# Kernel tuning notes

Measured on AMD Instinct MI355X. Metric: run time of the kernel, lower is better.

The kernel has to match this reference:

```python
import jax, jax.numpy as jnp
import numpy as np

VOCAB = 100000
DIM = 128
B = 16384
CTX = 10
NNEG = 10


def setup_inputs() -> dict:
    key = jax.random.key(0)
    k1, k2, k3, k4, k5 = jax.random.split(key, 5)
    initrange = 1.0 / DIM
    u_weight = jax.random.uniform(k1, (VOCAB, DIM), jnp.float32, -initrange, initrange)
    # original inits v to zeros; use small random so grads/score are non-trivial
    v_weight = jax.random.uniform(k2, (VOCAB, DIM), jnp.float32, -initrange, initrange)
    pos_u = jax.random.randint(k3, (B, CTX), 0, VOCAB)
    pos_v = jax.random.randint(k4, (B,), 0, VOCAB)
    neg_v = jax.random.randint(k5, (B, NNEG), 0, VOCAB)
    return {"pos_u": pos_u, "pos_v": pos_v, "neg_v": neg_v,
            "u_weight": u_weight, "v_weight": v_weight}


def reference(pos_u, pos_v, neg_v, u_weight, v_weight):
    # gather + mean over context: [B, D]
    emb_u = jnp.mean(u_weight[pos_u], axis=1)
    emb_v = v_weight[pos_v]              # [B, D]
    emb_neg_v = v_weight[neg_v]          # [B, N, D]

    score = jnp.sum(emb_u * emb_v, axis=1)          # [B]
    score = jnp.clip(score, -10.0, 10.0)
    score = -jax.nn.log_sigmoid(score)

    neg_score = jnp.einsum('bnd,bd->bn', emb_neg_v, emb_u)  # [B, N]
    neg_score = jnp.clip(neg_score, -10.0, 10.0)
    neg_score = -jnp.sum(jax.nn.log_sigmoid(-neg_score), axis=1)  # [B]

    return jnp.mean(score + neg_score)
```

## Files before the change

kernel.cpp:

```cpp
#include <hip/hip_runtime.h>
#include <math.h>

#define VOCAB 100000
#define DIM   128
#define BATCH 16384
#define CTX   10
#define NNEG  10

#define WAVES_PER_BLOCK 4
#define NBLOCKS (BATCH / WAVES_PER_BLOCK)

__device__ __forceinline__ float softplus_stable(float x) {
    return fmaxf(x, 0.0f) + log1pf(expf(-fabsf(x)));
}

__global__ __launch_bounds__(WAVES_PER_BLOCK * 64)
void cbow_loss_partial(const int* __restrict__ pos_u,
                       const int* __restrict__ pos_v,
                       const int* __restrict__ neg_v,
                       const float* __restrict__ u_weight,
                       const float* __restrict__ v_weight,
                       float* __restrict__ partial) {
    __shared__ float ls[WAVES_PER_BLOCK];

    const int tid  = threadIdx.x;
    const int wave = tid >> 6;
    const int lane = tid & 63;
    const int row  = blockIdx.x * WAVES_PER_BLOCK + wave;

    const int d2 = lane * 2;

    float2 acc = make_float2(0.0f, 0.0f);
    const int* pu = pos_u + row * CTX;
    #pragma unroll
    for (int c = 0; c < CTX; ++c) {
        const int idx = pu[c];
        const float2 u = *reinterpret_cast<const float2*>(
            u_weight + (size_t)idx * DIM + d2);
        acc.x += u.x;
        acc.y += u.y;
    }
    acc.x *= 0.1f;
    acc.y *= 0.1f;

    float p[1 + NNEG];
    {
        const int idx = pos_v[row];
        const float2 v = *reinterpret_cast<const float2*>(
            v_weight + (size_t)idx * DIM + d2);
        p[0] = acc.x * v.x + acc.y * v.y;
    }
    const int* nv = neg_v + row * NNEG;
    #pragma unroll
    for (int n = 0; n < NNEG; ++n) {
        const int idx = nv[n];
        const float2 v = *reinterpret_cast<const float2*>(
            v_weight + (size_t)idx * DIM + d2);
        p[1 + n] = acc.x * v.x + acc.y * v.y;
    }

    #pragma unroll
    for (int m = 32; m >= 1; m >>= 1) {
        #pragma unroll
        for (int k = 0; k < 1 + NNEG; ++k) {
            p[k] += __shfl_xor(p[k], m, 64);
        }
    }

    float s0 = fminf(fmaxf(p[0], -10.0f), 10.0f);
    float loss = softplus_stable(-s0);
    #pragma unroll
    for (int n = 0; n < NNEG; ++n) {
        float sn = fminf(fmaxf(p[1 + n], -10.0f), 10.0f);
        loss += softplus_stable(sn);
    }

    if (lane == 0) ls[wave] = loss;
    __syncthreads();
    if (tid == 0) {
        float blocksum = 0.0f;
        #pragma unroll
        for (int w = 0; w < WAVES_PER_BLOCK; ++w) blocksum += ls[w];
        partial[blockIdx.x] = blocksum;
    }
}

__global__ __launch_bounds__(1024)
void reduce_partials(const float* __restrict__ partial, float* __restrict__ out) {
    __shared__ float s[1024];
    const int tid = threadIdx.x;
    float v = partial[tid] + partial[tid + 1024] +
              partial[tid + 2048] + partial[tid + 3072];
    s[tid] = v;
    __syncthreads();
    #pragma unroll
    for (int ofs = 512; ofs >= 1; ofs >>= 1) {
        if (tid < ofs) s[tid] += s[tid + ofs];
        __syncthreads();
    }
    if (tid == 0) out[0] = s[0] * (1.0f / (float)BATCH);
}

extern "C" void kernel_launch(void* const* d_in, const int* in_sizes, int n_in,
                              void* d_out, int out_size, void* d_ws, size_t ws_size,
                              hipStream_t stream) {
    const int*   pos_u    = (const int*)d_in[0];
    const int*   pos_v    = (const int*)d_in[1];
    const int*   neg_v    = (const int*)d_in[2];
    const float* u_weight = (const float*)d_in[3];
    const float* v_weight = (const float*)d_in[4];
    float* out     = (float*)d_out;
    float* partial = (float*)d_ws;

    cbow_loss_partial<<<NBLOCKS, WAVES_PER_BLOCK * 64, 0, stream>>>(
        pos_u, pos_v, neg_v, u_weight, v_weight, partial);
    reduce_partials<<<1, 1024, 0, stream>>>(partial, out);
}
```

Before: 145.5 us.

## Hoist gather loads, scalarize indices, use DPP reductions and fast softplus

Rewrites the loss kernel. Row indices are loaded up front and made wave-uniform with readfirstlane, and all 21 embedding row loads are issued before any arithmetic so more memory requests are in flight. The shuffle-based lane reductions become DPP and ds_swizzle steps, and softplus switches to fast __expf/__logf intrinsics. Blocks grow to 8 waves, each wave writes its own partial with no block barrier, and the final reduction reads 16 values per thread followed by a wave reduction. Fast math slightly reduces accuracy, and the larger per-thread register footprint may lower occupancy.

```diff
diff --git a/kernel.cpp b/kernel.cpp
--- a/kernel.cpp
+++ b/kernel.cpp
@@ -1,104 +1,123 @@
 #include <hip/hip_runtime.h>
 #include <math.h>
 
-#define VOCAB 100000
 #define DIM   128
 #define BATCH 16384
 #define CTX   10
 #define NNEG  10
 
-#define WAVES_PER_BLOCK 4
-#define NBLOCKS (BATCH / WAVES_PER_BLOCK)
+#define WPB     8
+#define BLOCK   (WPB * 64)
+#define NBLOCKS (BATCH / WPB)
 
-__device__ __forceinline__ float softplus_stable(float x) {
-    return fmaxf(x, 0.0f) + log1pf(expf(-fabsf(x)));
+template <int CTRL>
+__device__ __forceinline__ float dpp_add(float v) {
+    int r = __builtin_amdgcn_mov_dpp(__float_as_int(v), CTRL, 0xF, 0xF, true);
+    return v + __int_as_float(r);
 }
 
-__global__ __launch_bounds__(WAVES_PER_BLOCK * 64)
-void cbow_loss_partial(const int* __restrict__ pos_u,
-                       const int* __restrict__ pos_v,
-                       const int* __restrict__ neg_v,
-                       const float* __restrict__ u_weight,
-                       const float* __restrict__ v_weight,
-                       float* __restrict__ partial) {
-    __shared__ float ls[WAVES_PER_BLOCK];
+__device__ __forceinline__ float wave_sum(float v) {
+    v = dpp_add<0xB1>(v);
+    v = dpp_add<0x4E>(v);
+    v = dpp_add<0x141>(v);
+    v = dpp_add<0x140>(v);
+    v += __int_as_float(__builtin_amdgcn_ds_swizzle(__float_as_int(v), 0x401F));
+    v += __shfl_xor(v, 32, 64);
+    return v;
+}
 
+__device__ __forceinline__ float softplus_fast(float x) {
+    return fmaxf(x, 0.0f) + __logf(1.0f + __expf(-fabsf(x)));
+}
+
+__global__ __launch_bounds__(BLOCK)
+void cbow_loss(const int* __restrict__ pos_u,
+               const int* __restrict__ pos_v,
+               const int* __restrict__ neg_v,
+               const float* __restrict__ u_weight,
+               const float* __restrict__ v_weight,
+               float* __restrict__ partial) {
     const int tid  = threadIdx.x;
     const int wave = tid >> 6;
     const int lane = tid & 63;
-    const int row  = blockIdx.x * WAVES_PER_BLOCK + wave;
+    const int row  = blockIdx.x * WPB + wave;
+    const int d2   = lane * 2;
 
-    const int d2 = lane * 2;
-
-    float2 acc = make_float2(0.0f, 0.0f);
+    int ui[CTX], vi[1 + NNEG];
     const int* pu = pos_u + row * CTX;
     #pragma unroll
-    for (int c = 0; c < CTX; ++c) {
-        const int idx = pu[c];
-        const float2 u = *reinterpret_cast<const float2*>(
-            u_weight + (size_t)idx * DIM + d2);
-        acc.x += u.x;
-        acc.y += u.y;
-    }
-    acc.x *= 0.1f;
-    acc.y *= 0.1f;
+    for (int c = 0; c < CTX; ++c)
+        ui[c] = __builtin_amdgcn_readfirstlane(pu[c]);
+    vi[0] = __builtin_amdgcn_readfirstlane(pos_v[row]);
+    const int* nv = neg_v + row * NNEG;
+    #pragma unroll
+    for (int n = 0; n < NNEG; ++n)
+        vi[1 + n] = __builtin_amdgcn_readfirstlane(nv[n]);
+
+    float2 uu[CTX];
+    #pragma unroll
+    for (int c = 0; c < CTX; ++c)
+        uu[c] = *reinterpret_cast<const float2*>(
+            u_weight + (size_t)ui[c] * DIM + d2);
+    float2 vv[1 + NNEG];
+    #pragma unroll
+    for (int k = 0; k < 1 + NNEG; ++k)
+        vv[k] = *reinterpret_cast<const float2*>(
+            v_weight + (size_t)vi[k] * DIM + d2);
+
+    float ax = 0.0f, ay = 0.0f;
+    #pragma unroll
+    for (int c = 0; c < CTX; ++c) { ax += uu[c].x; ay += uu[c].y; }
+    ax *= 0.1f; ay *= 0.1f;
 
     float p[1 + NNEG];
-    {
-        const int idx = pos_v[row];
-        const float2 v = *reinterpret_cast<const float2*>(
-            v_weight + (size_t)idx * DIM + d2);
-        p[0] = acc.x * v.x + acc.y * v.y;
-    }
-    const int* nv = neg_v + row * NNEG;
     #pragma unroll
-    for (int n = 0; n < NNEG; ++n) {
-        const int idx = nv[n];
-        const float2 v = *reinterpret_cast<const float2*>(
-            v_weight + (size_t)idx * DIM + d2);
-        p[1 + n] = acc.x * v.x + acc.y * v.y;
+    for (int k = 0; k < 1 + NNEG; ++k)
+        p[k] = ax * vv[k].x + ay * vv[k].y;
+
+    #pragma unroll
+    for (int k = 0; k < 1 + NNEG; ++k) p[k] = dpp_add<0xB1>(p[k]);
+    #pragma unroll
+    for (int k = 0; k < 1 + NNEG; ++k) p[k] = dpp_add<0x4E>(p[k]);
+    #pragma unroll
+    for (int k = 0; k < 1 + NNEG; ++k) p[k] = dpp_add<0x141>(p[k]);
+    #pragma unroll
+    for (int k = 0; k < 1 + NNEG; ++k) p[k] = dpp_add<0x140>(p[k]);
+    #pragma unroll
+    for (int k = 0; k < 1 + NNEG; ++k)
+        p[k] += __int_as_float(
+            __builtin_amdgcn_ds_swizzle(__float_as_int(p[k]), 0x401F));
+    #pragma unroll
+    for (int k = 0; k < 1 + NNEG; ++k) p[k] += __shfl_xor(p[k], 32, 64);
+
+    float s0   = fminf(fmaxf(p[0], -10.0f), 10.0f);
+    float loss = softplus_fast(-s0);
+    #pragma unroll
+    for (int n = 1; n <= NNEG; ++n) {
+        float sn = fminf(fmaxf(p[n], -10.0f), 10.0f);
+        loss += softplus_fast(sn);
     }
 
-    #pragma unroll
-    for (int m = 32; m >= 1; m >>= 1) {
-        #pragma unroll
-        for (int k = 0; k < 1 + NNEG; ++k) {
-            p[k] += __shfl_xor(p[k], m, 64);
-        }
-    }
-
-    float s0 = fminf(fmaxf(p[0], -10.0f), 10.0f);
-    float loss = softplus_stable(-s0);
-    #pragma unroll
-    for (int n = 0; n < NNEG; ++n) {
-        float sn = fminf(fmaxf(p[1 + n], -10.0f), 10.0f);
-        loss += softplus_stable(sn);
-    }
-
-    if (lane == 0) ls[wave] = loss;
-    __syncthreads();
-    if (tid == 0) {
-        float blocksum = 0.0f;
-        #pragma unroll
-        for (int w = 0; w < WAVES_PER_BLOCK; ++w) blocksum += ls[w];
-        partial[blockIdx.x] = blocksum;
-    }
+    if (lane == 0) partial[row] = loss;
 }
 
 __global__ __launch_bounds__(1024)
 void reduce_partials(const float* __restrict__ partial, float* __restrict__ out) {
-    __shared__ float s[1024];
     const int tid = threadIdx.x;
-    float v = partial[tid] + partial[tid + 1024] +
-              partial[tid + 2048] + partial[tid + 3072];
-    s[tid] = v;
+    float s = 0.0f;
+    #pragma unroll
+    for (int i = 0; i < BATCH / 1024; ++i)
+        s += partial[tid + i * 1024];
+    s = wave_sum(s);
+    __shared__ float ls[16];
+    if ((tid & 63) == 0) ls[tid >> 6] = s;
     __syncthreads();
-    #pragma unroll
-    for (int ofs = 512; ofs >= 1; ofs >>= 1) {
-        if (tid < ofs) s[tid] += s[tid + ofs];
-        __syncthreads();
+    if (tid == 0) {
+        float t = 0.0f;
+        #pragma unroll
+        for (int w = 0; w < 16; ++w) t += ls[w];
+        out[0] = t * (1.0f / (float)BATCH);
     }
-    if (tid == 0) out[0] = s[0] * (1.0f / (float)BATCH);
 }
 
 extern "C" void kernel_launch(void* const* d_in, const int* in_sizes, int n_in,
@@ -112,7 +131,7 @@
     float* out     = (float*)d_out;
     float* partial = (float*)d_ws;
 
-    cbow_loss_partial<<<NBLOCKS, WAVES_PER_BLOCK * 64, 0, stream>>>(
+    cbow_loss<<<NBLOCKS, BLOCK, 0, stream>>>(
         pos_u, pos_v, neg_v, u_weight, v_weight, partial);
     reduce_partials<<<1, 1024, 0, stream>>>(partial, out);
 }
```

Result: faster. 136.1 us (-6.5%).
